# Kernel tuning notes

Hardware: AMD Instinct MI355X
Metric: run time of the kernel (lower is better)

The kernel has to match this reference:

```python
import jax, jax.numpy as jnp
import numpy as np

T, N = 1024, 1024
DT = 0.5          # timestep used for velocity
DIS_THRESH = 12.0 # neighbor inclusion radius


def setup_inputs() -> dict:
    key = jax.random.key(0)
    ks = jax.random.split(key, 13)
    inp = {"a": jax.random.normal(ks[0], (T, N, 2), dtype=jnp.float32) * 10.0}
    # shared MLP (single linear layer) parameters
    inp["W1"] = jax.random.normal(ks[1], (1, 2), dtype=jnp.float32) * 0.5
    inp["b1"] = jax.random.normal(ks[2], (1,), dtype=jnp.float32) * 0.1
    inp["W2"] = jax.random.normal(ks[3], (1, 2), dtype=jnp.float32) * 0.5
    inp["b2"] = jax.random.normal(ks[4], (1,), dtype=jnp.float32) * 0.1
    inp["W3"] = jax.random.normal(ks[5], (1, 2), dtype=jnp.float32) * 0.5
    inp["b3"] = jax.random.normal(ks[6], (1,), dtype=jnp.float32) * 0.1
    inp["W4"] = jax.random.normal(ks[7], (1, 2), dtype=jnp.float32) * 0.5
    inp["b4"] = jax.random.normal(ks[8], (1,), dtype=jnp.float32) * 0.1
    inp["W5"] = jax.random.normal(ks[9], (1, 4), dtype=jnp.float32) * 0.5
    inp["b5"] = jax.random.normal(ks[10], (1,), dtype=jnp.float32) * 0.1
    inp["W6"] = jax.random.normal(ks[11], (64, 4), dtype=jnp.float32) * 0.5
    inp["b6"] = jax.random.normal(ks[12], (64,), dtype=jnp.float32) * 0.1
    return inp


def reference(a, W1, b1, W2, b2, W3, b3, W4, b4, W5, b5, W6, b6):
    # a: [T, N, 2]. Effective computation per (t in 1..T-1, node i),
    # neighbor j = N-1 (the inner qqq loop only keeps its last iteration).
    p = a[1:]              # [T-1, N, 2] current positions
    prev = a[:-1]          # [T-1, N, 2] previous positions
    pj = p[:, -1:, :]      # [T-1, 1, 2] neighbor (last node)

    dis = jnp.sqrt(jnp.sum((p - pj) ** 2, axis=-1))      # [T-1, N]
    d = p - prev                                          # displacement
    v = jnp.sqrt(jnp.sum(d ** 2, axis=-1)) / DT           # [T-1, N]
    ang = jnp.arctan2(d[..., 1], d[..., 0])               # [T-1, N]

    v_j = v[:, -1:]       # [T-1, 1]
    ang_j = ang[:, -1:]   # [T-1, 1]
    mask = (dis <= DIS_THRESH).astype(a.dtype)            # [T-1, N]

    def lin2(W, b, x0, x1):
        # 2-input linear; neighbor term masked out when dis > thresh
        return W[0, 0] * x0 + W[0, 1] * x1 + b[0]

    x_m = lin2(W1, b1, p[..., 0], mask * pj[..., 0])
    y_m = lin2(W2, b2, p[..., 1], mask * pj[..., 1])
    v_m = lin2(W3, b3, v, mask * v_j)
    a_m = lin2(W4, b4, ang, mask * ang_j)

    feat = jnp.stack([x_m, y_m, v_m, a_m], axis=-1)       # [T-1, N, 4]
    sss = jnp.einsum('tnf,of->tno', feat, W5) + b5        # [T-1, N, 1]
    sss64 = jnp.einsum('tnf,of->tno', feat, W6) + b6      # [T-1, N, 64]

    # node_out = [node[0]] + node : duplicate first computed timestep
    out1 = jnp.concatenate([sss[:1], sss], axis=0)        # [T, N, 1]
    out64 = jnp.concatenate([sss64[:1], sss64], axis=0)   # [T, N, 64]
    return out1, out64
```

## Files before the change

### kernel.cpp

```cpp
#include <hip/hip_runtime.h>

#define TT 1024
#define NN 1024
#define TS (TT - 1)

__global__ __launch_bounds__(256) void fused_traj_kernel(
    const float* __restrict__ a,
    const float* __restrict__ W1, const float* __restrict__ b1,
    const float* __restrict__ W2, const float* __restrict__ b2,
    const float* __restrict__ W3, const float* __restrict__ b3,
    const float* __restrict__ W4, const float* __restrict__ b4,
    const float* __restrict__ W5, const float* __restrict__ b5,
    const float* __restrict__ W6, const float* __restrict__ b6,
    float* __restrict__ out1, float* __restrict__ out64)
{
    __shared__ float sFeat[64 * 4];

    const int bid = blockIdx.x;
    const int ts  = bid >> 4;
    const int n0  = (bid & 15) << 6;
    const int tid = threadIdx.x;

    if (tid < 64) {
        const int n = n0 + tid;
        const float2* a2 = (const float2*)a;
        const float2 p   = a2[(size_t)(ts + 1) * NN + n];
        const float2 pr  = a2[(size_t)ts * NN + n];
        const float2 pj  = a2[(size_t)(ts + 1) * NN + (NN - 1)];
        const float2 prj = a2[(size_t)ts * NN + (NN - 1)];

        const float dx  = p.x - pj.x, dy = p.y - pj.y;
        const float dis = sqrtf(dx * dx + dy * dy);

        const float ddx = p.x - pr.x, ddy = p.y - pr.y;
        const float v   = sqrtf(ddx * ddx + ddy * ddy) * 2.0f;
        const float ang = atan2f(ddy, ddx);

        const float jdx = pj.x - prj.x, jdy = pj.y - prj.y;
        const float vj   = sqrtf(jdx * jdx + jdy * jdy) * 2.0f;
        const float angj = atan2f(jdy, jdx);

        const float mask = (dis <= 12.0f) ? 1.0f : 0.0f;

        const float x_m = W1[0] * p.x + W1[1] * (mask * pj.x) + b1[0];
        const float y_m = W2[0] * p.y + W2[1] * (mask * pj.y) + b2[0];
        const float v_m = W3[0] * v   + W3[1] * (mask * vj)   + b3[0];
        const float a_m = W4[0] * ang + W4[1] * (mask * angj) + b4[0];

        const float sss = W5[0] * x_m + W5[1] * y_m + W5[2] * v_m +
                          W5[3] * a_m + b5[0];

        out1[(size_t)(ts + 1) * NN + n] = sss;
        if (ts == 0) out1[n] = sss;

        sFeat[tid * 4 + 0] = x_m;
        sFeat[tid * 4 + 1] = y_m;
        sFeat[tid * 4 + 2] = v_m;
        sFeat[tid * 4 + 3] = a_m;
    }

    const int c0 = (tid * 4) & 63;
    float4 w6r[4];
    float  b6r[4];
#pragma unroll
    for (int k = 0; k < 4; ++k) {
        w6r[k] = ((const float4*)W6)[c0 + k];
        b6r[k] = b6[c0 + k];
    }

    __syncthreads();

    float* dst  = out64 + ((size_t)(ts + 1) * NN + n0) * 64;
    float* dst0 = out64 + (size_t)n0 * 64;

#pragma unroll
    for (int j = 0; j < 4; ++j) {
        const int pair = (tid >> 4) + 16 * j;
        const float4 ft = ((const float4*)sFeat)[pair];

        float4 o;
        o.x = ft.x * w6r[0].x + ft.y * w6r[0].y + ft.z * w6r[0].z + ft.w * w6r[0].w + b6r[0];
        o.y = ft.x * w6r[1].x + ft.y * w6r[1].y + ft.z * w6r[1].z + ft.w * w6r[1].w + b6r[1];
        o.z = ft.x * w6r[2].x + ft.y * w6r[2].y + ft.z * w6r[2].z + ft.w * w6r[2].w + b6r[2];
        o.w = ft.x * w6r[3].x + ft.y * w6r[3].y + ft.z * w6r[3].z + ft.w * w6r[3].w + b6r[3];

        const int f = pair * 64 + c0;
        *(float4*)(dst + f) = o;
        if (ts == 0) *(float4*)(dst0 + f) = o;
    }
}

extern "C" void kernel_launch(void* const* d_in, const int* in_sizes, int n_in,
                              void* d_out, int out_size, void* d_ws, size_t ws_size,
                              hipStream_t stream)
{
    const float* a  = (const float*)d_in[0];
    const float* W1 = (const float*)d_in[1];
    const float* b1 = (const float*)d_in[2];
    const float* W2 = (const float*)d_in[3];
    const float* b2 = (const float*)d_in[4];
    const float* W3 = (const float*)d_in[5];
    const float* b3 = (const float*)d_in[6];
    const float* W4 = (const float*)d_in[7];
    const float* b4 = (const float*)d_in[8];
    const float* W5 = (const float*)d_in[9];
    const float* b5 = (const float*)d_in[10];
    const float* W6 = (const float*)d_in[11];
    const float* b6 = (const float*)d_in[12];

    float* out1  = (float*)d_out;
    float* out64 = out1 + (size_t)TT * NN;

    const int grid = TS * (NN / 64);
    fused_traj_kernel<<<grid, 256, 0, stream>>>(
        a, W1, b1, W2, b2, W3, b3, W4, b4, W5, b5, W6, b6, out1, out64);
}
```

Measured before the change: 58.41 us.

## Process a full timestep row per block with nontemporal stores

Each block now handles all 1024 nodes of one output timestep, with block 0 recomputing timestep 1 instead of blocks at ts 0 issuing duplicate writes. The neighbor velocity and angle are computed once per block, and all 256 threads compute features rather than only 64. Outputs are written with nontemporal stores to cut cache pollution on the ~270MB write stream. The grid shrinks from ~16K to 1024 blocks with 16KB shared memory each, which may reduce latency hiding, and block 0 redundantly recomputes the first row.

```diff
diff --git a/kernel.cpp b/kernel.cpp
--- a/kernel.cpp
+++ b/kernel.cpp
@@ -2,9 +2,11 @@
 
 #define TT 1024
 #define NN 1024
-#define TS (TT - 1)
+#define BT 256
 
-__global__ __launch_bounds__(256) void fused_traj_kernel(
+typedef float v4f __attribute__((ext_vector_type(4)));
+
+__global__ __launch_bounds__(BT) void fused_traj_kernel(
     const float* __restrict__ a,
     const float* __restrict__ W1, const float* __restrict__ b1,
     const float* __restrict__ W2, const float* __restrict__ b2,
@@ -14,20 +16,25 @@
     const float* __restrict__ W6, const float* __restrict__ b6,
     float* __restrict__ out1, float* __restrict__ out64)
 {
-    __shared__ float sFeat[64 * 4];
+    __shared__ float sFeat[NN * 4];
 
-    const int bid = blockIdx.x;
-    const int ts  = bid >> 4;
-    const int n0  = (bid & 15) << 6;
+    const int b   = blockIdx.x;
+    const int rb  = (b == 0) ? 0 : b - 1;
     const int tid = threadIdx.x;
 
-    if (tid < 64) {
-        const int n = n0 + tid;
-        const float2* a2 = (const float2*)a;
-        const float2 p   = a2[(size_t)(ts + 1) * NN + n];
-        const float2 pr  = a2[(size_t)ts * NN + n];
-        const float2 pj  = a2[(size_t)(ts + 1) * NN + (NN - 1)];
-        const float2 prj = a2[(size_t)ts * NN + (NN - 1)];
+    const float2* a2 = (const float2*)a;
+
+    const float2 pj  = a2[(size_t)(rb + 1) * NN + (NN - 1)];
+    const float2 prj = a2[(size_t)rb * NN + (NN - 1)];
+    const float jdx = pj.x - prj.x, jdy = pj.y - prj.y;
+    const float vj   = sqrtf(jdx * jdx + jdy * jdy) * 2.0f;
+    const float angj = atan2f(jdy, jdx);
+
+#pragma unroll
+    for (int k = 0; k < 4; ++k) {
+        const int n = tid + BT * k;
+        const float2 p  = a2[(size_t)(rb + 1) * NN + n];
+        const float2 pr = a2[(size_t)rb * NN + n];
 
         const float dx  = p.x - pj.x, dy = p.y - pj.y;
         const float dis = sqrtf(dx * dx + dy * dy);
@@ -35,10 +42,6 @@
         const float ddx = p.x - pr.x, ddy = p.y - pr.y;
         const float v   = sqrtf(ddx * ddx + ddy * ddy) * 2.0f;
         const float ang = atan2f(ddy, ddx);
-
-        const float jdx = pj.x - prj.x, jdy = pj.y - prj.y;
-        const float vj   = sqrtf(jdx * jdx + jdy * jdy) * 2.0f;
-        const float angj = atan2f(jdy, jdx);
 
         const float mask = (dis <= 12.0f) ? 1.0f : 0.0f;
 
@@ -50,16 +53,15 @@
         const float sss = W5[0] * x_m + W5[1] * y_m + W5[2] * v_m +
                           W5[3] * a_m + b5[0];
 
-        out1[(size_t)(ts + 1) * NN + n] = sss;
-        if (ts == 0) out1[n] = sss;
+        __builtin_nontemporal_store(sss, &out1[(size_t)b * NN + n]);
 
-        sFeat[tid * 4 + 0] = x_m;
-        sFeat[tid * 4 + 1] = y_m;
-        sFeat[tid * 4 + 2] = v_m;
-        sFeat[tid * 4 + 3] = a_m;
+        sFeat[n * 4 + 0] = x_m;
+        sFeat[n * 4 + 1] = y_m;
+        sFeat[n * 4 + 2] = v_m;
+        sFeat[n * 4 + 3] = a_m;
     }
 
-    const int c0 = (tid * 4) & 63;
+    const int c0 = (tid & 15) * 4;
     float4 w6r[4];
     float  b6r[4];
 #pragma unroll
@@ -70,23 +72,20 @@
 
     __syncthreads();
 
-    float* dst  = out64 + ((size_t)(ts + 1) * NN + n0) * 64;
-    float* dst0 = out64 + (size_t)n0 * 64;
+    float* dst = out64 + (size_t)b * (NN * 64) + tid * 4;
+    const int a0 = tid >> 4;
 
-#pragma unroll
-    for (int j = 0; j < 4; ++j) {
-        const int pair = (tid >> 4) + 16 * j;
-        const float4 ft = ((const float4*)sFeat)[pair];
+#pragma unroll 8
+    for (int it = 0; it < 64; ++it) {
+        const float4 ft = ((const float4*)sFeat)[a0 + 16 * it];
 
-        float4 o;
+        v4f o;
         o.x = ft.x * w6r[0].x + ft.y * w6r[0].y + ft.z * w6r[0].z + ft.w * w6r[0].w + b6r[0];
         o.y = ft.x * w6r[1].x + ft.y * w6r[1].y + ft.z * w6r[1].z + ft.w * w6r[1].w + b6r[1];
         o.z = ft.x * w6r[2].x + ft.y * w6r[2].y + ft.z * w6r[2].z + ft.w * w6r[2].w + b6r[2];
         o.w = ft.x * w6r[3].x + ft.y * w6r[3].y + ft.z * w6r[3].z + ft.w * w6r[3].w + b6r[3];
 
-        const int f = pair * 64 + c0;
-        *(float4*)(dst + f) = o;
-        if (ts == 0) *(float4*)(dst0 + f) = o;
+        __builtin_nontemporal_store(o, (v4f*)(dst + (size_t)it * (BT * 4)));
     }
 }
 
@@ -111,7 +110,6 @@
     float* out1  = (float*)d_out;
     float* out64 = out1 + (size_t)TT * NN;
 
-    const int grid = TS * (NN / 64);
-    fused_traj_kernel<<<grid, 256, 0, stream>>>(
+    fused_traj_kernel<<<TT, BT, 0, stream>>>(
         a, W1, b1, W2, b2, W3, b3, W4, b4, W5, b5, W6, b6, out1, out64);
 }
```

After: 55.45 us. -5.1%, faster.
